# Kernel optimization log

Hardware: AMD Instinct MI355X
Metric: run time of the kernel (lower is better)

Reference implementation:

```python
import jax, jax.numpy as jnp
import numpy as np

L, H, F, FH, MLPD = 12, 12, 768, 64, 3072  # layers, heads, d_model, head_dim, mlp hidden
GH, GW = 32, 32
N = 1 + GH * GW  # cls token + patches
EPS = 1e-6
QK_SCALE = FH ** (-0.5)
STAGE_ENDS = (2, 5, 8, 11)  # last layer index of each of the 4 stages (3 layers/stage)


def _relpos_index(h, w):
    # standard timm BEiT relative position index with 3 extra cls entries
    coords = np.stack(np.meshgrid(np.arange(h), np.arange(w), indexing="ij"))  # 2,h,w
    cf = coords.reshape(2, -1)
    rel = (cf[:, :, None] - cf[:, None, :]).transpose(1, 2, 0).astype(np.int64)  # hw,hw,2
    rel[:, :, 0] += h - 1
    rel[:, :, 1] += w - 1
    rel[:, :, 0] *= 2 * w - 1
    num_rel = (2 * h - 1) * (2 * w - 1) + 3
    idx = np.zeros((h * w + 1, h * w + 1), dtype=np.int32)
    idx[1:, 1:] = rel.sum(-1)
    idx[0, 0:] = num_rel - 3
    idx[0:, 0] = num_rel - 2
    idx[0, 0] = num_rel - 1
    return idx, num_rel


def setup_inputs() -> dict:
    key = jax.random.key(0)
    ks = jax.random.split(key, 10)
    s = 0.02
    idx, R = _relpos_index(GH, GW)
    return dict(
        patch_tokens=jax.random.normal(ks[0], (1, GH * GW, F), jnp.float32),
        cls_token=jax.random.normal(ks[1], (1, 1, F), jnp.float32) * s,
        ln1_w=jnp.ones((L, F), jnp.float32),
        ln1_b=jnp.zeros((L, F), jnp.float32),
        qkv_w=jax.random.normal(ks[2], (L, 3 * F, F), jnp.float32) * s,
        q_bias=jax.random.normal(ks[3], (L, H, FH), jnp.float32) * s,
        v_bias=jax.random.normal(ks[4], (L, H, FH), jnp.float32) * s,
        proj_w=jax.random.normal(ks[5], (L, F, F), jnp.float32) * s,
        proj_b=jnp.zeros((L, F), jnp.float32),
        scale_attn=jnp.full((L, F), 0.1, jnp.float32),
        ln2_w=jnp.ones((L, F), jnp.float32),
        ln2_b=jnp.zeros((L, F), jnp.float32),
        fc1_w=jax.random.normal(ks[6], (L, MLPD, F), jnp.float32) * s,
        fc1_b=jnp.zeros((L, MLPD), jnp.float32),
        fc2_w=jax.random.normal(ks[7], (L, F, MLPD), jnp.float32) * s,
        fc2_b=jnp.zeros((L, F), jnp.float32),
        scale_mlp=jnp.full((L, F), 0.1, jnp.float32),
        relpos_table=jax.random.normal(ks[8], (L, R, H), jnp.float32) * s,
        relpos_index=jnp.asarray(idx),
        patch_grid_hw=jnp.array([GH, GW], jnp.int32),
    )


def _ln(x, w, b):
    mu = jnp.mean(x, -1, keepdims=True)
    var = jnp.mean(jnp.square(x - mu), -1, keepdims=True)
    return (x - mu) * jax.lax.rsqrt(var + EPS) * w + b


def reference(patch_tokens, cls_token, ln1_w, ln1_b, qkv_w, q_bias, v_bias,
              proj_w, proj_b, scale_attn, ln2_w, ln2_b, fc1_w, fc1_b, fc2_w,
              fc2_b, scale_mlp, relpos_table, relpos_index, patch_grid_hw):
    B = patch_tokens.shape[0]
    tokens = jnp.concatenate(
        [jnp.broadcast_to(cls_token, (B, 1, F)), patch_tokens], axis=1)  # B,N,F

    params = dict(ln1_w=ln1_w, ln1_b=ln1_b, qkv_w=qkv_w, q_bias=q_bias,
                  v_bias=v_bias, proj_w=proj_w, proj_b=proj_b,
                  scale_attn=scale_attn, ln2_w=ln2_w, ln2_b=ln2_b,
                  fc1_w=fc1_w, fc1_b=fc1_b, fc2_w=fc2_w, fc2_b=fc2_b,
                  scale_mlp=scale_mlp, relpos_table=relpos_table)

    def step(x, p):
        h = _ln(x, p['ln1_w'], p['ln1_b'])
        qkv = jnp.einsum('bnf,gf->bng', h, p['qkv_w'])          # B,N,3F (no bias)
        qkv = qkv.reshape(B, N, 3, H, FH).transpose(2, 0, 3, 1, 4)
        q, k, v = qkv[0], qkv[1], qkv[2]                         # B,H,N,fh
        q = (q + p['q_bias'][None, :, None, :]) * QK_SCALE
        v = v + p['v_bias'][None, :, None, :]
        bias = p['relpos_table'][relpos_index]                   # N,N,H
        attn = jnp.einsum('bhnd,bhmd->bhnm', q, k) + bias.transpose(2, 0, 1)[None]
        w = jax.nn.softmax(attn, axis=-1)
        o = jnp.einsum('bhnm,bhmd->bhnd', w, v).transpose(0, 2, 1, 3).reshape(B, N, F)
        o = o @ p['proj_w'].T + p['proj_b']
        x = x + p['scale_attn'] * o
        h2 = _ln(x, p['ln2_w'], p['ln2_b'])
        m = jax.nn.gelu(h2 @ p['fc1_w'].T + p['fc1_b'], approximate=False)
        m = m @ p['fc2_w'].T + p['fc2_b']
        x = x + p['scale_mlp'] * m
        return x, x

    _, ys = jax.lax.scan(step, tokens, params)  # ys: L,B,N,F
    return (ys[STAGE_ENDS[0]], ys[STAGE_ENDS[1]], ys[STAGE_ENDS[2]], ys[STAGE_ENDS[3]])
```

## Files before the change

### kernel.cpp

```cpp
#include <hip/hip_runtime.h>
#include <hip/hip_bf16.h>
#include <math.h>

#define L_LAYERS 12
#define H_HEADS  12
#define F_DIM    768
#define FH_DIM   64
#define MLPD     3072
#define NT       1025
#define NTP      1056
#define THREE_F  2304
#define R_REL    3972
#define QK_SCALE 0.125f
#define QB       64
#define KB       128

#define CQKV  (THREE_F * F_DIM)
#define CPROJ (F_DIM * F_DIM)
#define CFC1  (MLPD * F_DIM)
#define CFC2  (F_DIM * MLPD)

typedef short short8_t __attribute__((ext_vector_type(8)));
typedef float f32x4_t  __attribute__((ext_vector_type(4)));
typedef unsigned short u16x4_t __attribute__((ext_vector_type(4)));
typedef __attribute__((address_space(1))) const void* gptr_t;
typedef __attribute__((address_space(3))) void*       lptr_t;

typedef __hip_bfloat16 bf16;

static __device__ inline unsigned short f2bf(float f) {
    __hip_bfloat16 b(f);
    unsigned short u;
    __builtin_memcpy(&u, &b, 2);
    return u;
}

__device__ inline void xcd_remap(int& tx, int& ty) {
    int gx = gridDim.x, gy = gridDim.y;
    int b = blockIdx.y * gx + blockIdx.x;
    int total = gx * gy;
    int q = total >> 3, r = total & 7;
    int xcd = b & 7, i = b >> 3;
    int pos = (xcd < r) ? xcd * (q + 1) + i : r * (q + 1) + (xcd - r) * q + i;
    ty = pos / gx;
    tx = pos - ty * gx;
}

__global__ void setup_k(const float* __restrict__ patch, const float* __restrict__ cls,
                        const float* __restrict__ t,
                        float* __restrict__ x, bf16* __restrict__ vt,
                        float* __restrict__ tt) {
    const int E0 = NT * F_DIM;
    const int E1 = H_HEADS * FH_DIM * NTP;
    const int E3 = L_LAYERS * R_REL * H_HEADS;
    const int total = E0 + E1 + E3;
    for (int i = blockIdx.x * 256 + threadIdx.x; i < total; i += gridDim.x * 256) {
        if (i < E0) {
            int n = i / F_DIM, f = i - n * F_DIM;
            x[i] = (n == 0) ? cls[f] : patch[(size_t)(n - 1) * F_DIM + f];
        } else if (i < E0 + E1) {
            vt[i - E0] = __hip_bfloat16(0.0f);
        } else {
            int e = i - E0 - E1;
            int l = e / (R_REL * H_HEADS), rem = e - l * (R_REL * H_HEADS);
            int rr = rem / H_HEADS, hh = rem - rr * H_HEADS;
            tt[((size_t)l * H_HEADS + hh) * R_REL + rr] = t[e];
        }
    }
}

__global__ void conv_all_k(const float* __restrict__ qkv_w, const float* __restrict__ proj_w,
                           const float* __restrict__ fc1_w, const float* __restrict__ fc2_w,
                           bf16* __restrict__ wq, bf16* __restrict__ wp,
                           bf16* __restrict__ w1, bf16* __restrict__ w2) {
    const long A1 = (long)L_LAYERS * CQKV;
    const long A2 = A1 + (long)L_LAYERS * CPROJ;
    const long A3 = A2 + (long)L_LAYERS * CFC1;
    const long A4 = A3 + (long)L_LAYERS * CFC2;
    const long total4 = A4 >> 2;
    for (long qd = (long)blockIdx.x * 256 + threadIdx.x; qd < total4;
         qd += (long)gridDim.x * 256) {
        long e = qd << 2;
        const float* s; bf16* d; long off;
        if (e < A1)      { s = qkv_w;  d = wq; off = e; }
        else if (e < A2) { s = proj_w; d = wp; off = e - A1; }
        else if (e < A3) { s = fc1_w;  d = w1; off = e - A2; }
        else             { s = fc2_w;  d = w2; off = e - A3; }
        f32x4_t v = __builtin_nontemporal_load(reinterpret_cast<const f32x4_t*>(s + off));
        u16x4_t o;
        o.x = f2bf(v.x); o.y = f2bf(v.y); o.z = f2bf(v.z); o.w = f2bf(v.w);
        *reinterpret_cast<u16x4_t*>(d + off) = o;
    }
}

__global__ void layernorm_k(const float* __restrict__ x, const float* __restrict__ w,
                            const float* __restrict__ b, bf16* __restrict__ out) {
    const int row = blockIdx.x;
    const float* xr = x + (size_t)row * F_DIM;
    float v0 = xr[threadIdx.x];
    float v1 = xr[threadIdx.x + 256];
    float v2 = xr[threadIdx.x + 512];
    float s  = v0 + v1 + v2;
    float s2 = v0 * v0 + v1 * v1 + v2 * v2;
    #pragma unroll
    for (int off = 32; off; off >>= 1) {
        s  += __shfl_down(s, off);
        s2 += __shfl_down(s2, off);
    }
    __shared__ float ws_[4], ws2_[4];
    int lane = threadIdx.x & 63, wid = threadIdx.x >> 6;
    if (lane == 0) { ws_[wid] = s; ws2_[wid] = s2; }
    __syncthreads();
    float S  = ws_[0] + ws_[1] + ws_[2] + ws_[3];
    float S2 = ws2_[0] + ws2_[1] + ws2_[2] + ws2_[3];
    float mu  = S * (1.0f / F_DIM);
    float var = S2 * (1.0f / F_DIM) - mu * mu;
    float rs  = rsqrtf(var + 1e-6f);
    bf16* orow = out + (size_t)row * F_DIM;
    orow[threadIdx.x]       = __hip_bfloat16((v0 - mu) * rs * w[threadIdx.x]       + b[threadIdx.x]);
    orow[threadIdx.x + 256] = __hip_bfloat16((v1 - mu) * rs * w[threadIdx.x + 256] + b[threadIdx.x + 256]);
    orow[threadIdx.x + 512] = __hip_bfloat16((v2 - mu) * rs * w[threadIdx.x + 512] + b[threadIdx.x + 512]);
}

template <int T, int NLOAD>
__device__ inline void stage_glds(const bf16* __restrict__ g0, int ld, int rows_rem,
                                  bf16* lds, int tid) {
    #pragma unroll
    for (int i = 0; i < NLOAD; ++i) {
        int slot = i * T + tid;
        int row = slot >> 3, s = slot & 7;
        int grow = row < rows_rem ? row : (rows_rem - 1);
        const bf16* src = g0 + (size_t)grow * ld + ((s ^ (row & 7)) * 8);
        bf16* dst = lds + (size_t)(i * T + (tid & ~63)) * 8;
        __builtin_amdgcn_global_load_lds((gptr_t)src, (lptr_t)dst, 16, 0, 0);
    }
}

template <int EPI, int BM, int BN, int WM, int WN>
__global__ __launch_bounds__((BM / (WM * 16)) * (BN / (WN * 16)) * 64)
void gemm_k(const bf16* __restrict__ A, const bf16* __restrict__ B,
            int M, int Nc, int K, int lda, int ldb,
            const float* __restrict__ p0, const float* __restrict__ p1,
            float* __restrict__ outF, float* __restrict__ outDup,
            bf16* __restrict__ outB0, bf16* __restrict__ outB1, bf16* __restrict__ outB2) {
    constexpr int NWM = BM / (WM * 16);
    constexpr int NWN = BN / (WN * 16);
    constexpr int T   = NWM * NWN * 64;
    constexpr int ALOADS = BM * 8 / T;
    constexpr int BLOADS = BN * 8 / T;

    __shared__ __align__(16) bf16 As[2][BM * 64];
    __shared__ __align__(16) bf16 Bs[2][BN * 64];

    int tx, ty;
    xcd_remap(tx, ty);
    const int tid  = threadIdx.x;
    const int lane = tid & 63, wid = tid >> 6;
    const int wr = wid / NWN, wc = wid % NWN;
    const int g4 = lane >> 4, l16 = lane & 15;
    const int bm = tx * BM, bn = ty * BN;
    const bf16* Ab = A + (size_t)bm * lda;
    const bf16* Bb = B + (size_t)bn * ldb;
    const int aRows = min(BM, M - bm);
    const int bRows = min(BN, Nc - bn);

    f32x4_t acc[WM][WN] = {};
    const int NK = K >> 6;

    stage_glds<T, ALOADS>(Ab, lda, aRows, As[0], tid);
    stage_glds<T, BLOADS>(Bb, ldb, bRows, Bs[0], tid);
    __syncthreads();

    for (int t = 0; t < NK; ++t) {
        const int c = t & 1;
        if (t + 1 < NK) {
            stage_glds<T, ALOADS>(Ab + (t + 1) * 64, lda, aRows, As[c ^ 1], tid);
            stage_glds<T, BLOADS>(Bb + (t + 1) * 64, ldb, bRows, Bs[c ^ 1], tid);
        }
        const short* AsS = reinterpret_cast<const short*>(As[c]);
        const short* BsS = reinterpret_cast<const short*>(Bs[c]);
        #pragma unroll
        for (int kk = 0; kk < 2; ++kk) {
            short8_t af[WM], bfr[WN];
            #pragma unroll
            for (int mi = 0; mi < WM; ++mi) {
                int ar = wr * WM * 16 + mi * 16 + l16;
                int j = (kk * 4 + g4) ^ (ar & 7);
                af[mi] = *reinterpret_cast<const short8_t*>(AsS + ar * 64 + j * 8);
            }
            #pragma unroll
            for (int ni = 0; ni < WN; ++ni) {
                int br = wc * WN * 16 + ni * 16 + l16;
                int j = (kk * 4 + g4) ^ (br & 7);
                bfr[ni] = *reinterpret_cast<const short8_t*>(BsS + br * 64 + j * 8);
            }
            #pragma unroll
            for (int mi = 0; mi < WM; ++mi)
                #pragma unroll
                for (int ni = 0; ni < WN; ++ni)
                    acc[mi][ni] = __builtin_amdgcn_mfma_f32_16x16x32_bf16(
                        af[mi], bfr[ni], acc[mi][ni], 0, 0, 0);
        }
        __syncthreads();
    }

    #pragma unroll
    for (int mi = 0; mi < WM; ++mi) {
        #pragma unroll
        for (int r = 0; r < 4; ++r) {
            const int row = bm + wr * WM * 16 + mi * 16 + g4 * 4 + r;
            if (row >= M) continue;
            #pragma unroll
            for (int ni = 0; ni < WN; ++ni) {
                const int col = bn + wc * WN * 16 + ni * 16 + l16;
                float v = acc[mi][ni][r];
                if (EPI == 0) {
                    if (col < F_DIM) {
                        int h = col >> 6, d = col & 63;
                        float q = (v + p0[col]) * QK_SCALE;
                        outB0[((size_t)h * NT + row) * 64 + d] = __hip_bfloat16(q);
                    } else if (col < 2 * F_DIM) {
                        int g = col - F_DIM;
                        int h = g >> 6, d = g & 63;
                        outB1[((size_t)h * NT + row) * 64 + d] = __hip_bfloat16(v);
                    } else {
                        int g = col - 2 * F_DIM;
                        int h = g >> 6, d = g & 63;
                        float vv = v + p1[g];
                        outB2[((size_t)h * 64 + d) * NTP + row] = __hip_bfloat16(vv);
                    }
                } else if (EPI == 3) {
                    size_t oi = (size_t)row * Nc + col;
                    v += p0[col];
                    float nv = outF[oi] + p1[col] * v;
                    outF[oi] = nv;
                    if (outDup) outDup[oi] = nv;
                } else if (EPI == 4) {
                    v += p0[col];
                    float g = 0.5f * v * (1.0f + erff(v * 0.70710678118654752f));
                    outB0[(size_t)row * MLPD + col] = __hip_bfloat16(g);
                }
            }
        }
    }
}

__global__ __launch_bounds__(256)
void flash_k(const bf16* __restrict__ q_bf, const bf16* __restrict__ k_bf,
             const bf16* __restrict__ v_t,
             const float* __restrict__ tableT, bf16* __restrict__ o_bf) {
    __shared__ __align__(16) bf16 Qs[QB * 64];
    __shared__ __align__(16) bf16 Ks[2][KB * 64];
    __shared__ __align__(16) bf16 Vs[2][64 * KB];
    __shared__ __align__(16) bf16 Ps[4][16 * KB];

    int qx, h;
    xcd_remap(qx, h);
    const int tid = threadIdx.x, lane = tid & 63, w = tid >> 6;
    const int qb = qx * QB;
    const bf16* qh = q_bf + (size_t)h * NT * 64;
    const bf16* kh = k_bf + (size_t)h * NT * 64;
    const bf16* vh = v_t  + (size_t)h * 64 * NTP;
    const float* tbl = tableT + (size_t)h * R_REL;
    const int q_local = lane & 15;
    const int g4 = lane >> 4;

    auto stageKV = [&](int buf, int m0) {
        const int kRows = min(KB, NT - m0);
        #pragma unroll
        for (int i = 0; i < 4; ++i) {
            int slot = i * 256 + tid;
            int row = slot >> 3, s = slot & 7;
            int grow = min(row, kRows - 1);
            const bf16* src = kh + (size_t)(m0 + grow) * 64 + (s ^ (row & 7)) * 8;
            bf16* dst = Ks[buf] + (size_t)(i * 256 + (tid & ~63)) * 8;
            __builtin_amdgcn_global_load_lds((gptr_t)src, (lptr_t)dst, 16, 0, 0);
        }
        #pragma unroll
        for (int i = 0; i < 4; ++i) {
            int slot = i * 256 + tid;
            int d = slot >> 4, s = slot & 15;
            int msl = min(m0 / 8 + (s ^ (d & 15)), NTP / 8 - 1);
            const bf16* src = vh + (size_t)d * NTP + msl * 8;
            bf16* dst = Vs[buf] + (size_t)(i * 256 + (tid & ~63)) * 8;
            __builtin_amdgcn_global_load_lds((gptr_t)src, (lptr_t)dst, 16, 0, 0);
        }
    };

    {
        const int qRows = min(QB, NT - qb);
        #pragma unroll
        for (int i = 0; i < 2; ++i) {
            int slot = i * 256 + tid;
            int row = slot >> 3, s = slot & 7;
            int grow = min(row, qRows - 1);
            const bf16* src = qh + (size_t)(qb + grow) * 64 + (s ^ (row & 7)) * 8;
            bf16* dst = Qs + (size_t)(i * 256 + (tid & ~63)) * 8;
            __builtin_amdgcn_global_load_lds((gptr_t)src, (lptr_t)dst, 16, 0, 0);
        }
    }
    stageKV(0, 0);
    __syncthreads();

    short8_t qf[2];
    {
        const short* QsS = (const short*)Qs;
        #pragma unroll
        for (int kk = 0; kk < 2; ++kk) {
            int row = w * 16 + q_local;
            int slot = (kk * 4 + g4) ^ (row & 7);
            qf[kk] = *(const short8_t*)(QsS + row * 64 + slot * 8);
        }
    }

    const int qrow_base = qb + w * 16 + g4 * 4;
    int base_n[4]; bool nz[4];
    #pragma unroll
    for (int r = 0; r < 4; ++r) {
        int qc = min(qrow_base + r, NT - 1);
        nz[r] = (qc == 0);
        int p = qc - 1;
        base_n[r] = (p >> 5) * 63 + (p & 31) + 1984;
    }

    float m_run[4], l_run[4];
    f32x4_t acc[4] = {};
    #pragma unroll
    for (int r = 0; r < 4; ++r) { m_run[r] = -1e30f; l_run[r] = 0.0f; }

    const int NTILES = (NT + KB - 1) / KB;
    for (int t = 0; t < NTILES; ++t) {
        const int m0 = t * KB;
        const int c = t & 1;
        if (t + 1 < NTILES) stageKV(c ^ 1, (t + 1) * KB);

        f32x4_t sfr[8];
        {
            const short* KsS = (const short*)Ks[c];
            #pragma unroll
            for (int f = 0; f < 8; ++f) {
                f32x4_t cacc = {};
                #pragma unroll
                for (int kk = 0; kk < 2; ++kk) {
                    int mrow = f * 16 + q_local;
                    int slot = (kk * 4 + g4) ^ (mrow & 7);
                    short8_t bv = *(const short8_t*)(KsS + mrow * 64 + slot * 8);
                    cacc = __builtin_amdgcn_mfma_f32_16x16x32_bf16(qf[kk], bv, cacc, 0, 0, 0);
                }
                sfr[f] = cacc;
            }
        }

        #pragma unroll
        for (int f = 0; f < 8; ++f) {
            int mm = m0 + f * 16 + q_local;
            if (mm < NT) {
                if (mm == 0) {
                    #pragma unroll
                    for (int r = 0; r < 4; ++r)
                        sfr[f][r] += tbl[nz[r] ? 3971 : 3970];
                } else {
                    int pm = mm - 1;
                    int base_m = (pm >> 5) * 63 + (pm & 31);
                    #pragma unroll
                    for (int r = 0; r < 4; ++r) {
                        int idx = nz[r] ? 3969 : (base_n[r] - base_m);
                        sfr[f][r] += tbl[idx];
                    }
                }
            } else {
                #pragma unroll
                for (int r = 0; r < 4; ++r) sfr[f][r] = -1e30f;
            }
        }

        float pmax[4];
        #pragma unroll
        for (int r = 0; r < 4; ++r) {
            float mx = sfr[0][r];
            #pragma unroll
            for (int f = 1; f < 8; ++f) mx = fmaxf(mx, sfr[f][r]);
            pmax[r] = mx;
        }
        #pragma unroll
        for (int off = 1; off < 16; off <<= 1)
            #pragma unroll
            for (int r = 0; r < 4; ++r) pmax[r] = fmaxf(pmax[r], __shfl_xor(pmax[r], off));

        float fac[4];
        #pragma unroll
        for (int r = 0; r < 4; ++r) {
            float mnew = fmaxf(m_run[r], pmax[r]);
            fac[r] = __expf(m_run[r] - mnew);
            m_run[r] = mnew;
        }

        float rsum[4] = {0.f, 0.f, 0.f, 0.f};
        short* PsW = (short*)Ps[w];
        #pragma unroll
        for (int f = 0; f < 8; ++f) {
            int mloc = f * 16 + q_local;
            #pragma unroll
            for (int r = 0; r < 4; ++r) {
                int ql = g4 * 4 + r;
                float p = __expf(sfr[f][r] - m_run[r]);
                rsum[r] += p;
                PsW[ql * 128 + (((mloc >> 3) ^ ql) * 8) + (mloc & 7)] = (short)f2bf(p);
            }
        }
        #pragma unroll
        for (int off = 1; off < 16; off <<= 1)
            #pragma unroll
            for (int r = 0; r < 4; ++r) rsum[r] += __shfl_xor(rsum[r], off);
        #pragma unroll
        for (int r = 0; r < 4; ++r) l_run[r] = l_run[r] * fac[r] + rsum[r];
        #pragma unroll
        for (int df = 0; df < 4; ++df)
            #pragma unroll
            for (int r = 0; r < 4; ++r) acc[df][r] *= fac[r];

        {
            const short* PsR = (const short*)Ps[w];
            const short* VsS = (const short*)Vs[c];
            #pragma unroll
            for (int kk = 0; kk < 4; ++kk) {
                int j = kk * 4 + g4;
                short8_t pa = *(const short8_t*)(PsR + q_local * 128 + (j ^ q_local) * 8);
                #pragma unroll
                for (int df = 0; df < 4; ++df) {
                    int drow = df * 16 + q_local;
                    short8_t vb = *(const short8_t*)(VsS + drow * 128 + (j ^ (drow & 15)) * 8);
                    acc[df] = __builtin_amdgcn_mfma_f32_16x16x32_bf16(pa, vb, acc[df], 0, 0, 0);
                }
            }
        }
        __syncthreads();
    }

    #pragma unroll
    for (int df = 0; df < 4; ++df) {
        #pragma unroll
        for (int r = 0; r < 4; ++r) {
            int qq = qb + w * 16 + g4 * 4 + r;
            if (qq < NT) {
                float o = acc[df][r] / l_run[r];
                o_bf[(size_t)qq * F_DIM + h * 64 + df * 16 + q_local] = __hip_bfloat16(o);
            }
        }
    }
}

extern "C" void kernel_launch(void* const* d_in, const int* in_sizes, int n_in,
                              void* d_out, int out_size, void* d_ws, size_t ws_size,
                              hipStream_t stream) {
    const float* patch      = (const float*)d_in[0];
    const float* cls        = (const float*)d_in[1];
    const float* ln1_w      = (const float*)d_in[2];
    const float* ln1_b      = (const float*)d_in[3];
    const float* qkv_w      = (const float*)d_in[4];
    const float* q_bias     = (const float*)d_in[5];
    const float* v_bias     = (const float*)d_in[6];
    const float* proj_w     = (const float*)d_in[7];
    const float* proj_b     = (const float*)d_in[8];
    const float* scale_attn = (const float*)d_in[9];
    const float* ln2_w      = (const float*)d_in[10];
    const float* ln2_b      = (const float*)d_in[11];
    const float* fc1_w      = (const float*)d_in[12];
    const float* fc1_b      = (const float*)d_in[13];
    const float* fc2_w      = (const float*)d_in[14];
    const float* fc2_b      = (const float*)d_in[15];
    const float* scale_mlp  = (const float*)d_in[16];
    const float* table      = (const float*)d_in[17];
    float* out = (float*)d_out;

    char* ws = (char*)d_ws;
    size_t off = 0;
    auto alloc = [&](size_t bytes) { char* p = ws + off; off += (bytes + 255) & ~255ULL; return p; };

    float* x      = (float*)alloc((size_t)NT * F_DIM * 4);
    bf16*  h_bf   = (bf16*) alloc((size_t)NT * F_DIM * 2);
    bf16*  q_bf   = (bf16*) alloc((size_t)H_HEADS * NT * 64 * 2);
    bf16*  k_bf   = (bf16*) alloc((size_t)H_HEADS * NT * 64 * 2);
    bf16*  v_t    = (bf16*) alloc((size_t)H_HEADS * 64 * NTP * 2);
    bf16*  o_bf   = (bf16*) alloc((size_t)NT * F_DIM * 2);
    bf16*  m1_bf  = (bf16*) alloc((size_t)NT * MLPD * 2);
    float* tableT = (float*)alloc((size_t)L_LAYERS * H_HEADS * R_REL * 4);
    bf16*  wq_all = (bf16*) alloc((size_t)L_LAYERS * CQKV * 2);
    bf16*  wp_all = (bf16*) alloc((size_t)L_LAYERS * CPROJ * 2);
    bf16*  w1_all = (bf16*) alloc((size_t)L_LAYERS * CFC1 * 2);
    bf16*  w2_all = (bf16*) alloc((size_t)L_LAYERS * CFC2 * 2);

    setup_k<<<2048, 256, 0, stream>>>(patch, cls, table, x, v_t, tableT);
    conv_all_k<<<2048, 256, 0, stream>>>(qkv_w, proj_w, fc1_w, fc2_w,
                                         wq_all, wp_all, w1_all, w2_all);

    int stage = 0;
    for (int l = 0; l < L_LAYERS; ++l) {
        layernorm_k<<<NT, 256, 0, stream>>>(x, ln1_w + l * F_DIM, ln1_b + l * F_DIM, h_bf);

        gemm_k<0, 64, 128, 2, 2><<<dim3(17, 18), 512, 0, stream>>>(
            h_bf, wq_all + (size_t)l * CQKV, NT, THREE_F, F_DIM, F_DIM, F_DIM,
            q_bias + (size_t)l * F_DIM, v_bias + (size_t)l * F_DIM,
            nullptr, nullptr, q_bf, k_bf, v_t);

        flash_k<<<dim3((NT + QB - 1) / QB, H_HEADS), 256, 0, stream>>>(
            q_bf, k_bf, v_t,
            tableT + (size_t)l * H_HEADS * R_REL, o_bf);

        gemm_k<3, 32, 64, 1, 2><<<dim3(33, 12), 256, 0, stream>>>(
            o_bf, wp_all + (size_t)l * CPROJ, NT, F_DIM, F_DIM, F_DIM, F_DIM,
            proj_b + (size_t)l * F_DIM, scale_attn + (size_t)l * F_DIM,
            x, nullptr, nullptr, nullptr, nullptr);

        layernorm_k<<<NT, 256, 0, stream>>>(x, ln2_w + l * F_DIM, ln2_b + l * F_DIM, h_bf);

        gemm_k<4, 64, 128, 2, 2><<<dim3(17, 24), 512, 0, stream>>>(
            h_bf, w1_all + (size_t)l * CFC1, NT, MLPD, F_DIM, F_DIM, F_DIM,
            fc1_b + (size_t)l * MLPD, nullptr,
            nullptr, nullptr, m1_bf, nullptr, nullptr);

        const bool isStage = (l == 2 || l == 5 || l == 8 || l == 11);
        float* outDup = isStage ? (out + (size_t)stage * NT * F_DIM) : nullptr;
        gemm_k<3, 32, 64, 1, 2><<<dim3(33, 12), 256, 0, stream>>>(
            m1_bf, w2_all + (size_t)l * CFC2, NT, F_DIM, MLPD, MLPD, MLPD,
            fc2_b + (size_t)l * F_DIM, scale_mlp + (size_t)l * F_DIM,
            x, outDup, nullptr, nullptr, nullptr);
        if (isStage) ++stage;
    }
}
```

Baseline: 1.413 ms.

## Read Q/K/V fragments directly from global memory in flash attention, dropping LDS staging

Removes the shared-memory staging of Q, K and V tiles and the double-buffered async global-to-LDS loads in the attention kernel. Each wave now loads its MFMA operands straight from global memory (relying on L1/L2 caching) and the per-tile block barrier is removed. This cuts LDS footprint and synchronisation, but the four waves of a block each fetch the same K/V data separately and the loads lose their prefetch overlap with compute.

```diff
diff --git a/kernel.cpp b/kernel.cpp
--- a/kernel.cpp
+++ b/kernel.cpp
@@ -249,9 +249,6 @@
 void flash_k(const bf16* __restrict__ q_bf, const bf16* __restrict__ k_bf,
              const bf16* __restrict__ v_t,
              const float* __restrict__ tableT, bf16* __restrict__ o_bf) {
-    __shared__ __align__(16) bf16 Qs[QB * 64];
-    __shared__ __align__(16) bf16 Ks[2][KB * 64];
-    __shared__ __align__(16) bf16 Vs[2][64 * KB];
     __shared__ __align__(16) bf16 Ps[4][16 * KB];
 
     int qx, h;
@@ -265,52 +262,12 @@
     const int q_local = lane & 15;
     const int g4 = lane >> 4;
 
-    auto stageKV = [&](int buf, int m0) {
-        const int kRows = min(KB, NT - m0);
-        #pragma unroll
-        for (int i = 0; i < 4; ++i) {
-            int slot = i * 256 + tid;
-            int row = slot >> 3, s = slot & 7;
-            int grow = min(row, kRows - 1);
-            const bf16* src = kh + (size_t)(m0 + grow) * 64 + (s ^ (row & 7)) * 8;
-            bf16* dst = Ks[buf] + (size_t)(i * 256 + (tid & ~63)) * 8;
-            __builtin_amdgcn_global_load_lds((gptr_t)src, (lptr_t)dst, 16, 0, 0);
-        }
-        #pragma unroll
-        for (int i = 0; i < 4; ++i) {
-            int slot = i * 256 + tid;
-            int d = slot >> 4, s = slot & 15;
-            int msl = min(m0 / 8 + (s ^ (d & 15)), NTP / 8 - 1);
-            const bf16* src = vh + (size_t)d * NTP + msl * 8;
-            bf16* dst = Vs[buf] + (size_t)(i * 256 + (tid & ~63)) * 8;
-            __builtin_amdgcn_global_load_lds((gptr_t)src, (lptr_t)dst, 16, 0, 0);
-        }
-    };
-
-    {
-        const int qRows = min(QB, NT - qb);
-        #pragma unroll
-        for (int i = 0; i < 2; ++i) {
-            int slot = i * 256 + tid;
-            int row = slot >> 3, s = slot & 7;
-            int grow = min(row, qRows - 1);
-            const bf16* src = qh + (size_t)(qb + grow) * 64 + (s ^ (row & 7)) * 8;
-            bf16* dst = Qs + (size_t)(i * 256 + (tid & ~63)) * 8;
-            __builtin_amdgcn_global_load_lds((gptr_t)src, (lptr_t)dst, 16, 0, 0);
-        }
-    }
-    stageKV(0, 0);
-    __syncthreads();
-
     short8_t qf[2];
     {
-        const short* QsS = (const short*)Qs;
-        #pragma unroll
-        for (int kk = 0; kk < 2; ++kk) {
-            int row = w * 16 + q_local;
-            int slot = (kk * 4 + g4) ^ (row & 7);
-            qf[kk] = *(const short8_t*)(QsS + row * 64 + slot * 8);
-        }
+        int qrow = min(qb + w * 16 + q_local, NT - 1);
+        const bf16* qr = qh + (size_t)qrow * 64 + g4 * 8;
+        qf[0] = *reinterpret_cast<const short8_t*>(qr);
+        qf[1] = *reinterpret_cast<const short8_t*>(qr + 32);
     }
 
     const int qrow_base = qb + w * 16 + g4 * 4;
@@ -331,24 +288,18 @@
     const int NTILES = (NT + KB - 1) / KB;
     for (int t = 0; t < NTILES; ++t) {
         const int m0 = t * KB;
-        const int c = t & 1;
-        if (t + 1 < NTILES) stageKV(c ^ 1, (t + 1) * KB);
 
         f32x4_t sfr[8];
-        {
-            const short* KsS = (const short*)Ks[c];
-            #pragma unroll
-            for (int f = 0; f < 8; ++f) {
-                f32x4_t cacc = {};
-                #pragma unroll
-                for (int kk = 0; kk < 2; ++kk) {
-                    int mrow = f * 16 + q_local;
-                    int slot = (kk * 4 + g4) ^ (mrow & 7);
-                    short8_t bv = *(const short8_t*)(KsS + mrow * 64 + slot * 8);
-                    cacc = __builtin_amdgcn_mfma_f32_16x16x32_bf16(qf[kk], bv, cacc, 0, 0, 0);
-                }
-                sfr[f] = cacc;
-            }
+        #pragma unroll
+        for (int f = 0; f < 8; ++f) {
+            int mrow = min(m0 + f * 16 + q_local, NT - 1);
+            const bf16* kr = kh + (size_t)mrow * 64 + g4 * 8;
+            f32x4_t cacc = {};
+            cacc = __builtin_amdgcn_mfma_f32_16x16x32_bf16(
+                qf[0], *reinterpret_cast<const short8_t*>(kr), cacc, 0, 0, 0);
+            cacc = __builtin_amdgcn_mfma_f32_16x16x32_bf16(
+                qf[1], *reinterpret_cast<const short8_t*>(kr + 32), cacc, 0, 0, 0);
+            sfr[f] = cacc;
         }
 
         #pragma unroll
@@ -421,20 +372,20 @@
 
         {
             const short* PsR = (const short*)Ps[w];
-            const short* VsS = (const short*)Vs[c];
             #pragma unroll
             for (int kk = 0; kk < 4; ++kk) {
                 int j = kk * 4 + g4;
                 short8_t pa = *(const short8_t*)(PsR + q_local * 128 + (j ^ q_local) * 8);
+                int col8 = min(m0 / 8 + j, NTP / 8 - 1);
                 #pragma unroll
                 for (int df = 0; df < 4; ++df) {
                     int drow = df * 16 + q_local;
-                    short8_t vb = *(const short8_t*)(VsS + drow * 128 + (j ^ (drow & 15)) * 8);
+                    short8_t vb = *reinterpret_cast<const short8_t*>(
+                        vh + (size_t)drow * NTP + col8 * 8);
                     acc[df] = __builtin_amdgcn_mfma_f32_16x16x32_bf16(pa, vb, acc[df], 0, 0, 0);
                 }
             }
         }
-        __syncthreads();
     }
 
     #pragma unroll
```

New measurement: 1.666 ms. +17.9%, slower.
